# Kernel tuning notes

Hardware: AMD Instinct MI355X
Metric: run time of the kernel (lower is better)

The kernel has to match this reference:

```python
import jax, jax.numpy as jnp
import numpy as np

C64 = jnp.complex64


def _ry(t):  # scalar angle -> [2,2] complex
    c = jnp.cos(t / 2).astype(C64)
    s = jnp.sin(t / 2).astype(C64)
    return jnp.stack([jnp.stack([c, -s]), jnp.stack([s, c])])


def _rz(t):  # scalar angle -> [2,2] complex (diagonal)
    p = jnp.exp(-0.5j * t.astype(C64))
    z = jnp.zeros((), C64)
    return jnp.stack([jnp.stack([p, z]), jnp.stack([z, jnp.conj(p)])])


def _rx_batch(t):  # t: [B] -> [B,2,2] complex (per-sample RX encoding gate)
    c = jnp.cos(t / 2).astype(C64)
    s = jnp.sin(t / 2).astype(C64)
    row0 = jnp.stack([c, -1j * s], axis=-1)
    row1 = jnp.stack([-1j * s, c], axis=-1)
    return jnp.stack([row0, row1], axis=-2)


def _apply_1q(state, gate, wire, n):
    # state: [B, 2^n]; wire 0 is the most significant bit (PennyLane convention)
    B = state.shape[0]
    pre, post = 2 ** wire, 2 ** (n - wire - 1)
    s = state.reshape(B, pre, 2, post)
    if gate.ndim == 2:
        s = jnp.einsum('ij,bpjq->bpiq', gate, s)
    else:  # per-sample gate [B,2,2]
        s = jnp.einsum('bij,bpjq->bpiq', gate, s)
    return s.reshape(B, -1)


def _apply_cnot(state, wire, n):
    # CNOT with control=wire, target=wire+1 (adjacent wires)
    B = state.shape[0]
    pre, post = 2 ** wire, 2 ** (n - wire - 2)
    s = state.reshape(B, pre, 2, 2, post)
    # control==1 block gets its target axis flipped
    s = jnp.concatenate([s[:, :, :1], s[:, :, 1:, ::-1]], axis=2)
    return s.reshape(B, -1)


def _circuit(x, params):
    # Batched statevector simulation of: RX(x_i) encoding, then n_layers of
    # (RY,RZ,RY) per wire + CNOT chain, then <Z_i> per wire.
    B, n = x.shape
    L = params.shape[0]
    state = jnp.zeros((B, 2 ** n), C64).at[:, 0].set(1.0)
    for i in range(n):
        state = _apply_1q(state, _rx_batch(x[:, i]), i, n)
    for l in range(L):
        for i in range(n):
            # RY(p0) first, then RZ(p1), then RY(p2): fuse into one 2x2 gate
            g = _ry(params[l, i, 2]) @ _rz(params[l, i, 1]) @ _ry(params[l, i, 0])
            state = _apply_1q(state, g, i, n)
        for i in range(n - 1):
            state = _apply_cnot(state, i, n)
    probs = jnp.abs(state) ** 2  # [B, 2^n] float32
    ez = []
    for i in range(n):
        p = probs.reshape(B, 2 ** i, 2, 2 ** (n - i - 1))
        ez.append(p[:, :, 0].sum((1, 2)) - p[:, :, 1].sum((1, 2)))
    return jnp.stack(ez, axis=1)  # [B, n]


def setup_inputs() -> dict:
    key = jax.random.key(0)
    k1, k2, k3, _ = jax.random.split(key, 4)
    B, n, L = 8192, 12, 3
    return {
        'x': jax.random.normal(k1, (B, n), jnp.float32),
        'params': jax.random.normal(k2, (L, n, 3), jnp.float32),
        'head_w': jax.random.normal(k3, (1, n), jnp.float32) / np.float32(np.sqrt(n)),
        'head_b': jnp.zeros((1,), jnp.float32),
    }


def reference(x, params, head_w, head_b):
    ez = _circuit(x, params)           # [B, n] per-wire Z expectations
    out = ez @ head_w.T + head_b       # Linear(n, 1)
    return out[:, 0]                   # squeeze(-1) -> [B]
```

## Files before the change

kernel.cpp:

```cpp
#include <hip/hip_runtime.h>
#include <math.h>

#define NQ 12
#define NTH 256
#define NL 3
#define GRID 512

typedef _Float16 h8 __attribute__((ext_vector_type(8)));
typedef _Float16 h4 __attribute__((ext_vector_type(4)));
typedef float f4 __attribute__((ext_vector_type(4)));

#define MFMA __builtin_amdgcn_mfma_f32_16x16x32_f16


__device__ __forceinline__ int sfx(int v) {
    v ^= v >> 1; v ^= v >> 2; v ^= v >> 4; v ^= v >> 8;
    return v;
}
__device__ __forceinline__ int swzf(int off) {
    return off ^ (((((off >> 6) ^ (off >> 9)) & 7)) << 3);
}
__device__ __forceinline__ int swz1(int off) {
    return off ^ ((((off >> 5) ^ (off >> 9)) & 7) << 3);
}
__device__ __forceinline__ int swzw(int off) {
    return off ^ (((off >> 6) & 7) << 3);
}

__device__ __forceinline__ unsigned pk2(float lo, float hi) {
    auto t_ = __builtin_amdgcn_cvt_pkrtz(lo, hi);
    unsigned r_; __builtin_memcpy(&r_, &t_, 4); return r_;
}

__device__ __forceinline__ h8 xition(f4 re, f4 im) {
    unsigned a0 = pk2(re.x, re.y), a1 = pk2(re.z, re.w);
    unsigned b0 = pk2(im.x, im.y), b1 = pk2(im.z, im.w);
    asm("v_permlane32_swap_b32 %0, %1" : "+v"(a0), "+v"(b0));
    asm("v_permlane16_swap_b32 %0, %1" : "+v"(a0), "+v"(b0));
    asm("v_permlane32_swap_b32 %0, %1" : "+v"(a1), "+v"(b1));
    asm("v_permlane16_swap_b32 %0, %1" : "+v"(a1), "+v"(b1));
    union { unsigned u[4]; h8 v; } r_;
    r_.u[0] = a0; r_.u[1] = a1; r_.u[2] = b0; r_.u[3] = b1;
    return r_.v;
}

__global__ void __launch_bounds__(NTH, 3)
qsim_kernel(const float* __restrict__ x,
            const float* __restrict__ params,
            const float* __restrict__ head_w,
            const float* __restrict__ head_b,
            float* __restrict__ out, int Btot) {
    __shared__ __align__(16) _Float16 Sst[16384];
    __shared__ __align__(16) _Float16 Wl[6144];
    __shared__ float wlo[64], whi[64];
    __shared__ float csx[8 * 24], snx[8 * 24];
    __shared__ float Gs0[96];
    __shared__ __align__(16) float fct[2][48][2];
    __shared__ float wred[8];
    float* Gs = (float*)Sst;

    const int t = threadIdx.x, blk = blockIdx.x;
    const int npairs = (Btot + 1) >> 1;

    if (t < 36) {
        float p0 = params[t * 3 + 0], p1 = params[t * 3 + 1], p2 = params[t * 3 + 2];
        float c0 = cosf(0.5f * p0), s0 = sinf(0.5f * p0);
        float ch = cosf(0.5f * p1), sh = sinf(0.5f * p1);
        float c2 = cosf(0.5f * p2), s2 = sinf(0.5f * p2);
        float pr_ = ch, pi = -sh, qr = ch, qi = sh;
        float A = c2 * c0, Bc = s2 * s0, Cc = c2 * s0, D = s2 * c0;
        float* g = &Gs[t * 8];
        g[0] = A * pr_ - Bc * qr;  g[1] = A * pi - Bc * qi;
        g[2] = -Cc * pr_ - D * qr; g[3] = -Cc * pi - D * qi;
        g[4] = D * pr_ + Cc * qr;  g[5] = D * pi + Cc * qi;
        g[6] = -Bc * pr_ + A * qr; g[7] = -Bc * pi + A * qi;
    }
    if (t < 64) {
        int v = t; float s = 0.f, s2 = 0.f;
#pragma unroll
        for (int be = 0; be < 6; ++be) {
            s  += ((v >> be) & 1) ? -head_w[11 - be] : head_w[11 - be];
            s2 += ((v >> be) & 1) ? -head_w[5 - be]  : head_w[5 - be];
        }
        wlo[v] = s; whi[v] = s2;
    }
    if (t >= 64) {
        int idx = t - 64;
        int pr = idx / 24, w = idx - pr * 24;
        int pairIdx = blk + pr * GRID;
        if (pairIdx < npairs) {
            int smp = pairIdx * 2 + (w >= 12 ? 1 : 0);
            int wire = (w >= 12) ? (w - 12) : w;
            if (smp < Btot) {
                float xv = 0.5f * x[smp * NQ + wire];
                csx[pr * 24 + w] = cosf(xv);
                snx[pr * 24 + w] = sinf(xv);
            }
        }
    }
    __syncthreads();

    if (t < 96) Gs0[t] = Gs[t];
#pragma unroll
    for (int i = 0; i < 24; ++i) {
        int e = i * 256 + t;
        int s = (e >> 10) + 3;
        int idx = e & 1023;
        int n = idx >> 5, k = idx & 31;
        int rp = n >> 4, tp = n & 15, rr = k >> 4, tt = k & 15;
        int l = s / 3, g = s - 3 * l;
        float ur = 1.f, ui = 0.f;
#pragma unroll
        for (int jj = 0; jj < 4; ++jj) {
            int wire = 11 - (4 * g + jj);
            const float* gp = &Gs[(l * 12 + wire) * 8];
            int rb = (tp >> jj) & 1, cb = (tt >> jj) & 1;
            float gr = gp[(rb * 2 + cb) * 2], gi = gp[(rb * 2 + cb) * 2 + 1];
            float nr = ur * gr - ui * gi;
            float ni = ur * gi + ui * gr;
            ur = nr; ui = ni;
        }
        float val = (rp == 0) ? ((rr == 0) ? ur : -ui)
                              : ((rr == 0) ? ui : ur);
        Wl[swzw(e)] = (_Float16)val;
    }
    __syncthreads();

    const int wv = t >> 6, u = t & 15, q = (t >> 4) & 3;
    const int wbs = swzw(u * 32 + q * 8);
    int g0b[4], g1b[4];
#pragma unroll
    for (int mb = 0; mb < 4; ++mb) {
        int m_ = wv * 64 + (u >> 2) * 16 + mb * 4 + (u & 3);
        g0b[mb] = swzf(m_ * 32 + q * 8);
        int l_ = t & 63;
        int m1 = ((l_ >> 2) & 3) * 64 + (l_ & 3) * 16 + wv * 4 + mb;
        g1b[mb] = swz1(m1 * 32 + q * 8);
    }
    const int sb = (t * 32) ^ (((t ^ (t >> 4)) & 7) << 3);

    const int s4 = (u ^ (u >> 1) ^ (u >> 2) ^ (u >> 3)) & 15;
    const int P4 = s4 & 1, q0 = q & 1, q1 = q >> 1;
    const int j7 = q1 ^ P4, j6 = q0 ^ q1 ^ P4;
    const int wv0 = wv & 1, wv1 = wv >> 1;
    int Eo[4], PwR[4];
#pragma unroll
    for (int r = 0; r < 4; ++r) {
        int r0 = r & 1, r1 = r >> 1;
        int j5 = r1 ^ j6, j4 = (r0 ^ r1) ^ j6;
        int j3 = wv1 ^ j4, j2 = wv0 ^ wv1 ^ j4;
        int m0 = s4 * 16 + j7 * 8 + j6 * 4 + j5 * 2 + j4;
        Eo[r]  = swzf(m0 * 32 + j3 * 8 + j2 * 4);
        PwR[r] = (wv0 ^ wv1 ^ j4);
    }
    const int Pw0 = wv0 ^ wv1 ^ j6;
    const int wloB = j6 * 48 + (wv1 ^ j6) * 8 + (wv0 ^ wv1 ^ j6) * 4 + Pw0 * 3;
    const float whiv = whi[s4 * 4 + j7 * 2 + j6];
    const f4 Z = {0.f, 0.f, 0.f, 0.f};

    const int iu = (t ^ (t >> 1)) & 0xFF;
    const int aI = iu >> 4;
    const int bI = 16 + (iu & 15);
    const int flip = (t & 1) << 3;

#define ST16(off_, va_, vb_) {                                               \
    union { unsigned u[4]; h8 v; } w_;                                       \
    w_.u[0] = pk2((va_).x, (va_).y); w_.u[1] = pk2((va_).z, (va_).w);        \
    w_.u[2] = pk2((vb_).x, (vb_).y); w_.u[3] = pk2((vb_).z, (vb_).w);        \
    *(h8*)&Sst[off_] = w_.v; }

#define PST1(CMP_, r_) {                                                     \
    bool pw_ = PwR[r_] != 0;                                                 \
    { float v0=eRA[0].CMP_, v1=eRA[1].CMP_, v2=eRA[2].CMP_, v3=eRA[3].CMP_;  \
      float a0_=pw_?v2:v0, a1_=pw_?v3:v1, a2_=pw_?v1:v3, a3_=pw_?v0:v2;      \
      union { unsigned u[2]; h4 v; } w_;                                     \
      w_.u[0]=pk2(a0_,a1_); w_.u[1]=pk2(a2_,a3_);                            \
      *(h4*)&Sst[Eo[r_]] = w_.v; }                                           \
    { float v0=eIA[0].CMP_, v1=eIA[1].CMP_, v2=eIA[2].CMP_, v3=eIA[3].CMP_;  \
      float a0_=pw_?v2:v0, a1_=pw_?v3:v1, a2_=pw_?v1:v3, a3_=pw_?v0:v2;      \
      union { unsigned u[2]; h4 v; } w_;                                     \
      w_.u[0]=pk2(a0_,a1_); w_.u[1]=pk2(a2_,a3_);                            \
      *(h4*)&Sst[Eo[r_] ^ 16] = w_.v; }                                      \
    { float v0=eRB[0].CMP_, v1=eRB[1].CMP_, v2=eRB[2].CMP_, v3=eRB[3].CMP_;  \
      float a0_=pw_?v2:v0, a1_=pw_?v3:v1, a2_=pw_?v1:v3, a3_=pw_?v0:v2;      \
      union { unsigned u[2]; h4 v; } w_;                                     \
      w_.u[0]=pk2(a0_,a1_); w_.u[1]=pk2(a2_,a3_);                            \
      *(h4*)&Sst[Eo[r_] + 8192] = w_.v; }                                    \
    { float v0=eIB[0].CMP_, v1=eIB[1].CMP_, v2=eIB[2].CMP_, v3=eIB[3].CMP_;  \
      float a0_=pw_?v2:v0, a1_=pw_?v3:v1, a2_=pw_?v1:v3, a3_=pw_?v0:v2;      \
      union { unsigned u[2]; h4 v; } w_;                                     \
      w_.u[0]=pk2(a0_,a1_); w_.u[1]=pk2(a2_,a3_);                            \
      *(h4*)&Sst[(Eo[r_] ^ 16) + 8192] = w_.v; } }

#define RD1(CMP_, dr_) {                                                     \
    int b_ = wloB ^ (dr_);                                                   \
    float w0_ = whiv + wlo[b_],     w1_ = whiv + wlo[b_ ^ 1];                \
    float w2_ = whiv + wlo[b_ ^ 3], w3_ = whiv + wlo[b_ ^ 2];                \
    racc0 = fmaf(fmaf(eRA[0].CMP_, eRA[0].CMP_, eIA[0].CMP_*eIA[0].CMP_), w0_, racc0); \
    racc0 = fmaf(fmaf(eRA[1].CMP_, eRA[1].CMP_, eIA[1].CMP_*eIA[1].CMP_), w1_, racc0); \
    racc0 = fmaf(fmaf(eRA[2].CMP_, eRA[2].CMP_, eIA[2].CMP_*eIA[2].CMP_), w2_, racc0); \
    racc0 = fmaf(fmaf(eRA[3].CMP_, eRA[3].CMP_, eIA[3].CMP_*eIA[3].CMP_), w3_, racc0); \
    racc1 = fmaf(fmaf(eRB[0].CMP_, eRB[0].CMP_, eIB[0].CMP_*eIB[0].CMP_), w0_, racc1); \
    racc1 = fmaf(fmaf(eRB[1].CMP_, eRB[1].CMP_, eIB[1].CMP_*eIB[1].CMP_), w1_, racc1); \
    racc1 = fmaf(fmaf(eRB[2].CMP_, eRB[2].CMP_, eIB[2].CMP_*eIB[2].CMP_), w2_, racc1); \
    racc1 = fmaf(fmaf(eRB[3].CMP_, eRB[3].CMP_, eIB[3].CMP_*eIB[3].CMP_), w3_, racc1); }

#pragma unroll 1
    for (int pr = 0; ; ++pr) {
        const int pairIdx = blk + pr * GRID;
        if (pairIdx >= npairs) break;

        if (t < 96) {
            int s_ = t / 48, k_ = t - s_ * 48;
            int grp = k_ >> 4, h = k_ & 15;
            int wbase = (grp == 0) ? 3 : (grp == 1) ? 7 : 11;
            const float* cs_ = &csx[pr * 24 + s_ * 12];
            const float* sn_ = &snx[pr * 24 + s_ * 12];
            float ur = 1.f, ui = 0.f;
#pragma unroll
            for (int jj = 0; jj < 4; ++jj) {
                int w = wbase - jj;
                int bit = (h >> jj) & 1;
                const float* g = &Gs0[w * 8];
                float c = cs_[w], sn = sn_[w];
                float tr, ti;
                if (bit == 0) { tr = g[0] * c + g[3] * sn; ti = g[1] * c - g[2] * sn; }
                else          { tr = g[4] * c + g[7] * sn; ti = g[5] * c - g[6] * sn; }
                float nr = ur * tr - ui * ti, ni = ur * ti + ui * tr;
                ur = nr; ui = ni;
            }
            fct[s_][k_][0] = ur; fct[s_][k_][1] = ui;
        }
        __syncthreads();

#pragma unroll
        for (int s_ = 0; s_ < 2; ++s_) {
            const int SOFF = s_ * 8192;
            float ar = fct[s_][aI][0], ai = fct[s_][aI][1];
            float br = fct[s_][bI][0], bi = fct[s_][bI][1];
            float abr = ar * br - ai * bi, abi = ar * bi + ai * br;
            float cr[16], ci[16];
#pragma unroll
            for (int k = 0; k < 16; ++k) {
                cr[k] = fct[s_][32 + (k ^ flip)][0];
                ci[k] = fct[s_][32 + (k ^ flip)][1];
            }
            float vr_[16], vi_[16];
#pragma unroll
            for (int tau = 0; tau < 16; ++tau) {
                const int cidx = tau ^ (tau >> 1);
                vr_[tau] = abr * cr[cidx] - abi * ci[cidx];
                vi_[tau] = abr * ci[cidx] + abi * cr[cidx];
            }
            union { unsigned u[4]; h8 v; } R0_, R1_, I0_, I1_;
#pragma unroll
            for (int k = 0; k < 4; ++k) {
                R0_.u[k] = pk2(vr_[2 * k],     vr_[2 * k + 1]);
                R1_.u[k] = pk2(vr_[8 + 2 * k], vr_[8 + 2 * k + 1]);
                I0_.u[k] = pk2(vi_[2 * k],     vi_[2 * k + 1]);
                I1_.u[k] = pk2(vi_[8 + 2 * k], vi_[8 + 2 * k + 1]);
            }
            const int off0 = t * 32;
            *(h8*)&Sst[swzf(off0)      + SOFF] = R0_.v;
            *(h8*)&Sst[swzf(off0 + 8)  + SOFF] = R1_.v;
            *(h8*)&Sst[swzf(off0 + 16) + SOFF] = I0_.v;
            *(h8*)&Sst[swzf(off0 + 24) + SOFF] = I1_.v;
        }

        float racc0 = 0.f, racc1 = 0.f;
#pragma unroll
        for (int l = 1; l < NL; ++l) {
            {
                const int sW = ((l - 1) * 3 + 0) * 1024;
                h8 bf0 = *(const h8*)&Wl[sW + wbs];
                h8 bf1 = *(const h8*)&Wl[sW + 512 + wbs];
                h8 aA[4], aB[4];
#pragma unroll
                for (int mb = 0; mb < 4; ++mb) {
                    aA[mb] = *(const h8*)&Sst[g0b[mb]];
                    aB[mb] = *(const h8*)&Sst[g0b[mb] + 8192];
                }
                f4 cR[4], cI[4];
#pragma unroll
                for (int mb = 0; mb < 4; ++mb) {
                    cR[mb] = MFMA(aA[mb], bf0, Z, 0, 0, 0);
                    cI[mb] = MFMA(aA[mb], bf1, Z, 0, 0, 0);
                }
                ST16(sb,        cR[0], cR[1]) ST16(sb ^ 8,  cR[2], cR[3])
                ST16(sb ^ 16,   cI[0], cI[1]) ST16(sb ^ 24, cI[2], cI[3])
#pragma unroll
                for (int mb = 0; mb < 4; ++mb) {
                    cR[mb] = MFMA(aB[mb], bf0, Z, 0, 0, 0);
                    cI[mb] = MFMA(aB[mb], bf1, Z, 0, 0, 0);
                }
                ST16(sb + 8192,        cR[0], cR[1]) ST16((sb ^ 8) + 8192,  cR[2], cR[3])
                ST16((sb ^ 16) + 8192, cI[0], cI[1]) ST16((sb ^ 24) + 8192, cI[2], cI[3])
                __syncthreads();
            }
            {
                const int sW1 = ((l - 1) * 3 + 1) * 1024, sW2 = ((l - 1) * 3 + 2) * 1024;
                h8 bg0 = *(const h8*)&Wl[sW1 + wbs];
                h8 bg1 = *(const h8*)&Wl[sW1 + 512 + wbs];
                h8 bh0 = *(const h8*)&Wl[sW2 + wbs];
                h8 bh1 = *(const h8*)&Wl[sW2 + 512 + wbs];
                h8 gA[4], gB[4];
#pragma unroll
                for (int mb = 0; mb < 4; ++mb) {
                    gA[mb] = *(const h8*)&Sst[g1b[mb]];
                    gB[mb] = *(const h8*)&Sst[g1b[mb] + 8192];
                }
                if (l < NL - 1) __syncthreads();
                f4 eRA[4], eIA[4], eRB[4], eIB[4];
                {
                    f4 dR[4], dI[4]; h8 t2[4];
#pragma unroll
                    for (int mb = 0; mb < 4; ++mb) {
                        dR[mb] = MFMA(gA[mb], bg0, Z, 0, 0, 0);
                        dI[mb] = MFMA(gA[mb], bg1, Z, 0, 0, 0);
                    }
#pragma unroll
                    for (int mb = 0; mb < 4; ++mb) t2[mb] = xition(dR[mb], dI[mb]);
#pragma unroll
                    for (int mb = 0; mb < 4; ++mb) {
                        eRA[mb] = MFMA(t2[mb], bh0, Z, 0, 0, 0);
                        eIA[mb] = MFMA(t2[mb], bh1, Z, 0, 0, 0);
                    }
                }
                {
                    f4 dR[4], dI[4]; h8 t2[4];
#pragma unroll
                    for (int mb = 0; mb < 4; ++mb) {
                        dR[mb] = MFMA(gB[mb], bg0, Z, 0, 0, 0);
                        dI[mb] = MFMA(gB[mb], bg1, Z, 0, 0, 0);
                    }
#pragma unroll
                    for (int mb = 0; mb < 4; ++mb) t2[mb] = xition(dR[mb], dI[mb]);
#pragma unroll
                    for (int mb = 0; mb < 4; ++mb) {
                        eRB[mb] = MFMA(t2[mb], bh0, Z, 0, 0, 0);
                        eIB[mb] = MFMA(t2[mb], bh1, Z, 0, 0, 0);
                    }
                }
                if (l < NL - 1) {
                    PST1(x, 0) PST1(y, 1) PST1(z, 2) PST1(w, 3)
                    __syncthreads();
                } else {
                    RD1(x, 0) RD1(y, 31) RD1(z, 63) RD1(w, 32)
                }
            }
        }
#pragma unroll
        for (int o = 32; o >= 1; o >>= 1) {
            racc0 += __shfl_xor(racc0, o, 64);
            racc1 += __shfl_xor(racc1, o, 64);
        }
        if ((t & 63) == 0) { wred[wv] = racc0; wred[4 + wv] = racc1; }
        __syncthreads();
        if (t < 2) {
            int smp = pairIdx * 2 + t;
            if (smp < Btot) {
                float r = head_b[0];
#pragma unroll
                for (int i2 = 0; i2 < 4; ++i2) r += wred[t * 4 + i2];
                out[smp] = r;
            }
        }
    }
}

extern "C" void kernel_launch(void* const* d_in, const int* in_sizes, int n_in,
                              void* d_out, int out_size, void* d_ws, size_t ws_size,
                              hipStream_t stream) {
    const float* x = (const float*)d_in[0];
    const float* params = (const float*)d_in[1];
    const float* head_w = (const float*)d_in[2];
    const float* head_b = (const float*)d_in[3];
    float* out = (float*)d_out;
    int B = in_sizes[0] / NQ;

    hipLaunchKernelGGL(qsim_kernel, dim3(GRID), dim3(NTH), 0, stream,
                       x, params, head_w, head_b, out, B);
}
```

Measured before the change: 107.3 us.

## Process one sample per block iteration instead of two, doubling grid

Each block iteration now simulates a single sample's statevector instead of a pair. This halves shared memory for the state buffer and roughly halves register use, and the launch bound is raised to 4 blocks per CU with twice as many blocks in the grid. The aim is higher occupancy and better latency hiding. The cost is losing the interleaving of two independent MFMA chains per wave and paying the per-iteration barriers and setup once per sample instead of once per pair.

```diff
diff --git a/kernel.cpp b/kernel.cpp
--- a/kernel.cpp
+++ b/kernel.cpp
@@ -4,7 +4,7 @@
 #define NQ 12
 #define NTH 256
 #define NL 3
-#define GRID 512
+#define GRID 1024
 
 typedef _Float16 h8 __attribute__((ext_vector_type(8)));
 typedef _Float16 h4 __attribute__((ext_vector_type(4)));
@@ -44,23 +44,22 @@
     return r_.v;
 }
 
-__global__ void __launch_bounds__(NTH, 3)
+__global__ void __launch_bounds__(NTH, 4)
 qsim_kernel(const float* __restrict__ x,
             const float* __restrict__ params,
             const float* __restrict__ head_w,
             const float* __restrict__ head_b,
             float* __restrict__ out, int Btot) {
-    __shared__ __align__(16) _Float16 Sst[16384];
+    __shared__ __align__(16) _Float16 Sst[8192];
     __shared__ __align__(16) _Float16 Wl[6144];
     __shared__ float wlo[64], whi[64];
-    __shared__ float csx[8 * 24], snx[8 * 24];
+    __shared__ float csx[8 * 12], snx[8 * 12];
     __shared__ float Gs0[96];
-    __shared__ __align__(16) float fct[2][48][2];
-    __shared__ float wred[8];
+    __shared__ __align__(16) float fct[48][2];
+    __shared__ float wred[4];
     float* Gs = (float*)Sst;
 
     const int t = threadIdx.x, blk = blockIdx.x;
-    const int npairs = (Btot + 1) >> 1;
 
     if (t < 36) {
         float p0 = params[t * 3 + 0], p1 = params[t * 3 + 1], p2 = params[t * 3 + 2];
@@ -84,18 +83,14 @@
         }
         wlo[v] = s; whi[v] = s2;
     }
-    if (t >= 64) {
+    if (t >= 64 && t < 160) {
         int idx = t - 64;
-        int pr = idx / 24, w = idx - pr * 24;
-        int pairIdx = blk + pr * GRID;
-        if (pairIdx < npairs) {
-            int smp = pairIdx * 2 + (w >= 12 ? 1 : 0);
-            int wire = (w >= 12) ? (w - 12) : w;
-            if (smp < Btot) {
-                float xv = 0.5f * x[smp * NQ + wire];
-                csx[pr * 24 + w] = cosf(xv);
-                snx[pr * 24 + w] = sinf(xv);
-            }
+        int pr = idx / 12, w = idx - pr * 12;
+        int smp = blk + pr * GRID;
+        if (smp < Btot) {
+            float xv = 0.5f * x[smp * NQ + w];
+            csx[pr * 12 + w] = cosf(xv);
+            snx[pr * 12 + w] = sinf(xv);
         }
     }
     __syncthreads();
@@ -180,17 +175,7 @@
       float a0_=pw_?v2:v0, a1_=pw_?v3:v1, a2_=pw_?v1:v3, a3_=pw_?v0:v2;      \
       union { unsigned u[2]; h4 v; } w_;                                     \
       w_.u[0]=pk2(a0_,a1_); w_.u[1]=pk2(a2_,a3_);                            \
-      *(h4*)&Sst[Eo[r_] ^ 16] = w_.v; }                                      \
-    { float v0=eRB[0].CMP_, v1=eRB[1].CMP_, v2=eRB[2].CMP_, v3=eRB[3].CMP_;  \
-      float a0_=pw_?v2:v0, a1_=pw_?v3:v1, a2_=pw_?v1:v3, a3_=pw_?v0:v2;      \
-      union { unsigned u[2]; h4 v; } w_;                                     \
-      w_.u[0]=pk2(a0_,a1_); w_.u[1]=pk2(a2_,a3_);                            \
-      *(h4*)&Sst[Eo[r_] + 8192] = w_.v; }                                    \
-    { float v0=eIB[0].CMP_, v1=eIB[1].CMP_, v2=eIB[2].CMP_, v3=eIB[3].CMP_;  \
-      float a0_=pw_?v2:v0, a1_=pw_?v3:v1, a2_=pw_?v1:v3, a3_=pw_?v0:v2;      \
-      union { unsigned u[2]; h4 v; } w_;                                     \
-      w_.u[0]=pk2(a0_,a1_); w_.u[1]=pk2(a2_,a3_);                            \
-      *(h4*)&Sst[(Eo[r_] ^ 16) + 8192] = w_.v; } }
+      *(h4*)&Sst[Eo[r_] ^ 16] = w_.v; } }
 
 #define RD1(CMP_, dr_) {                                                     \
     int b_ = wloB ^ (dr_);                                                   \
@@ -199,23 +184,19 @@
     racc0 = fmaf(fmaf(eRA[0].CMP_, eRA[0].CMP_, eIA[0].CMP_*eIA[0].CMP_), w0_, racc0); \
     racc0 = fmaf(fmaf(eRA[1].CMP_, eRA[1].CMP_, eIA[1].CMP_*eIA[1].CMP_), w1_, racc0); \
     racc0 = fmaf(fmaf(eRA[2].CMP_, eRA[2].CMP_, eIA[2].CMP_*eIA[2].CMP_), w2_, racc0); \
-    racc0 = fmaf(fmaf(eRA[3].CMP_, eRA[3].CMP_, eIA[3].CMP_*eIA[3].CMP_), w3_, racc0); \
-    racc1 = fmaf(fmaf(eRB[0].CMP_, eRB[0].CMP_, eIB[0].CMP_*eIB[0].CMP_), w0_, racc1); \
-    racc1 = fmaf(fmaf(eRB[1].CMP_, eRB[1].CMP_, eIB[1].CMP_*eIB[1].CMP_), w1_, racc1); \
-    racc1 = fmaf(fmaf(eRB[2].CMP_, eRB[2].CMP_, eIB[2].CMP_*eIB[2].CMP_), w2_, racc1); \
-    racc1 = fmaf(fmaf(eRB[3].CMP_, eRB[3].CMP_, eIB[3].CMP_*eIB[3].CMP_), w3_, racc1); }
+    racc0 = fmaf(fmaf(eRA[3].CMP_, eRA[3].CMP_, eIA[3].CMP_*eIA[3].CMP_), w3_, racc0); }
 
 #pragma unroll 1
     for (int pr = 0; ; ++pr) {
-        const int pairIdx = blk + pr * GRID;
-        if (pairIdx >= npairs) break;
-
-        if (t < 96) {
-            int s_ = t / 48, k_ = t - s_ * 48;
+        const int smp = blk + pr * GRID;
+        if (smp >= Btot) break;
+
+        if (t < 48) {
+            int k_ = t;
             int grp = k_ >> 4, h = k_ & 15;
             int wbase = (grp == 0) ? 3 : (grp == 1) ? 7 : 11;
-            const float* cs_ = &csx[pr * 24 + s_ * 12];
-            const float* sn_ = &snx[pr * 24 + s_ * 12];
+            const float* cs_ = &csx[pr * 12];
+            const float* sn_ = &snx[pr * 12];
             float ur = 1.f, ui = 0.f;
 #pragma unroll
             for (int jj = 0; jj < 4; ++jj) {
@@ -229,21 +210,19 @@
                 float nr = ur * tr - ui * ti, ni = ur * ti + ui * tr;
                 ur = nr; ui = ni;
             }
-            fct[s_][k_][0] = ur; fct[s_][k_][1] = ui;
+            fct[k_][0] = ur; fct[k_][1] = ui;
         }
         __syncthreads();
 
-#pragma unroll
-        for (int s_ = 0; s_ < 2; ++s_) {
-            const int SOFF = s_ * 8192;
-            float ar = fct[s_][aI][0], ai = fct[s_][aI][1];
-            float br = fct[s_][bI][0], bi = fct[s_][bI][1];
+        {
+            float ar = fct[aI][0], ai = fct[aI][1];
+            float br = fct[bI][0], bi = fct[bI][1];
             float abr = ar * br - ai * bi, abi = ar * bi + ai * br;
             float cr[16], ci[16];
 #pragma unroll
             for (int k = 0; k < 16; ++k) {
-                cr[k] = fct[s_][32 + (k ^ flip)][0];
-                ci[k] = fct[s_][32 + (k ^ flip)][1];
+                cr[k] = fct[32 + (k ^ flip)][0];
+                ci[k] = fct[32 + (k ^ flip)][1];
             }
             float vr_[16], vi_[16];
 #pragma unroll
@@ -261,40 +240,31 @@
                 I1_.u[k] = pk2(vi_[8 + 2 * k], vi_[8 + 2 * k + 1]);
             }
             const int off0 = t * 32;
-            *(h8*)&Sst[swzf(off0)      + SOFF] = R0_.v;
-            *(h8*)&Sst[swzf(off0 + 8)  + SOFF] = R1_.v;
-            *(h8*)&Sst[swzf(off0 + 16) + SOFF] = I0_.v;
-            *(h8*)&Sst[swzf(off0 + 24) + SOFF] = I1_.v;
-        }
-
-        float racc0 = 0.f, racc1 = 0.f;
+            *(h8*)&Sst[swzf(off0)]      = R0_.v;
+            *(h8*)&Sst[swzf(off0 + 8)]  = R1_.v;
+            *(h8*)&Sst[swzf(off0 + 16)] = I0_.v;
+            *(h8*)&Sst[swzf(off0 + 24)] = I1_.v;
+        }
+
+        float racc0 = 0.f;
 #pragma unroll
         for (int l = 1; l < NL; ++l) {
             {
                 const int sW = ((l - 1) * 3 + 0) * 1024;
                 h8 bf0 = *(const h8*)&Wl[sW + wbs];
                 h8 bf1 = *(const h8*)&Wl[sW + 512 + wbs];
-                h8 aA[4], aB[4];
-#pragma unroll
-                for (int mb = 0; mb < 4; ++mb) {
+                h8 aA[4];
+#pragma unroll
+                for (int mb = 0; mb < 4; ++mb)
                     aA[mb] = *(const h8*)&Sst[g0b[mb]];
-                    aB[mb] = *(const h8*)&Sst[g0b[mb] + 8192];
-                }
                 f4 cR[4], cI[4];
 #pragma unroll
                 for (int mb = 0; mb < 4; ++mb) {
                     cR[mb] = MFMA(aA[mb], bf0, Z, 0, 0, 0);
                     cI[mb] = MFMA(aA[mb], bf1, Z, 0, 0, 0);
                 }
-                ST16(sb,        cR[0], cR[1]) ST16(sb ^ 8,  cR[2], cR[3])
-                ST16(sb ^ 16,   cI[0], cI[1]) ST16(sb ^ 24, cI[2], cI[3])
-#pragma unroll
-                for (int mb = 0; mb < 4; ++mb) {
-                    cR[mb] = MFMA(aB[mb], bf0, Z, 0, 0, 0);
-                    cI[mb] = MFMA(aB[mb], bf1, Z, 0, 0, 0);
-                }
-                ST16(sb + 8192,        cR[0], cR[1]) ST16((sb ^ 8) + 8192,  cR[2], cR[3])
-                ST16((sb ^ 16) + 8192, cI[0], cI[1]) ST16((sb ^ 24) + 8192, cI[2], cI[3])
+                ST16(sb,      cR[0], cR[1]) ST16(sb ^ 8,  cR[2], cR[3])
+                ST16(sb ^ 16, cI[0], cI[1]) ST16(sb ^ 24, cI[2], cI[3])
                 __syncthreads();
             }
             {
@@ -303,14 +273,12 @@
                 h8 bg1 = *(const h8*)&Wl[sW1 + 512 + wbs];
                 h8 bh0 = *(const h8*)&Wl[sW2 + wbs];
                 h8 bh1 = *(const h8*)&Wl[sW2 + 512 + wbs];
-                h8 gA[4], gB[4];
-#pragma unroll
-                for (int mb = 0; mb < 4; ++mb) {
+                h8 gA[4];
+#pragma unroll
+                for (int mb = 0; mb < 4; ++mb)
                     gA[mb] = *(const h8*)&Sst[g1b[mb]];
-                    gB[mb] = *(const h8*)&Sst[g1b[mb] + 8192];
-                }
                 if (l < NL - 1) __syncthreads();
-                f4 eRA[4], eIA[4], eRB[4], eIB[4];
+                f4 eRA[4], eIA[4];
                 {
                     f4 dR[4], dI[4]; h8 t2[4];
 #pragma unroll
@@ -324,21 +292,6 @@
                     for (int mb = 0; mb < 4; ++mb) {
                         eRA[mb] = MFMA(t2[mb], bh0, Z, 0, 0, 0);
                         eIA[mb] = MFMA(t2[mb], bh1, Z, 0, 0, 0);
-                    }
-                }
-                {
-                    f4 dR[4], dI[4]; h8 t2[4];
-#pragma unroll
-                    for (int mb = 0; mb < 4; ++mb) {
-                        dR[mb] = MFMA(gB[mb], bg0, Z, 0, 0, 0);
-                        dI[mb] = MFMA(gB[mb], bg1, Z, 0, 0, 0);
-                    }
-#pragma unroll
-                    for (int mb = 0; mb < 4; ++mb) t2[mb] = xition(dR[mb], dI[mb]);
-#pragma unroll
-                    for (int mb = 0; mb < 4; ++mb) {
-                        eRB[mb] = MFMA(t2[mb], bh0, Z, 0, 0, 0);
-                        eIB[mb] = MFMA(t2[mb], bh1, Z, 0, 0, 0);
                     }
                 }
                 if (l < NL - 1) {
@@ -350,20 +303,15 @@
             }
         }
 #pragma unroll
-        for (int o = 32; o >= 1; o >>= 1) {
+        for (int o = 32; o >= 1; o >>= 1)
             racc0 += __shfl_xor(racc0, o, 64);
-            racc1 += __shfl_xor(racc1, o, 64);
-        }
-        if ((t & 63) == 0) { wred[wv] = racc0; wred[4 + wv] = racc1; }
+        if ((t & 63) == 0) wred[wv] = racc0;
         __syncthreads();
-        if (t < 2) {
-            int smp = pairIdx * 2 + t;
-            if (smp < Btot) {
-                float r = head_b[0];
-#pragma unroll
-                for (int i2 = 0; i2 < 4; ++i2) r += wred[t * 4 + i2];
-                out[smp] = r;
-            }
+        if (t == 0) {
+            float r = head_b[0];
+#pragma unroll
+            for (int i2 = 0; i2 < 4; ++i2) r += wred[i2];
+            out[smp] = r;
         }
     }
 }
```

Measured after the change: 104.9 us. -2.2%, faster.
